# Performance work log

Hardware: AMD Instinct MI355X
Metric: run time of the kernel (lower is better)

The kernel has to match this reference:

```python
import jax, jax.numpy as jnp
import numpy as np

N_EMBED = 1024
HIDDEN = int(2 / 3 * 4 * N_EMBED)  # 2730, matches SwiGLU default
NUM_EXPERTS = 8
TOP_K = 2


def setup_inputs() -> dict:
    key = jax.random.key(0)
    ks = jax.random.split(key, 5)
    B, T, C, E, H = 2, 2048, N_EMBED, NUM_EXPERTS, HIDDEN
    s = 0.02
    return {
        "x": jax.random.normal(ks[0], (B, T, C), dtype=jnp.float32),
        "gate_w": jax.random.normal(ks[1], (E, C), dtype=jnp.float32) * s,  # Linear(C->E) weight [out,in]
        "w1": jax.random.normal(ks[2], (E, H, C), dtype=jnp.float32) * s,   # per-expert Linear(C->H)
        "w2": jax.random.normal(ks[3], (E, H, C), dtype=jnp.float32) * s,   # per-expert Linear(C->H)
        "w3": jax.random.normal(ks[4], (E, C, H), dtype=jnp.float32) * s,   # per-expert Linear(H->C)
    }


def reference(x, gate_w, w1, w2, w3):
    B, T, C = x.shape
    E = gate_w.shape[0]
    xt = x.reshape(-1, C)                      # [N, C], N = B*T
    N = xt.shape[0]

    # Router: top-k logits, softmax over the selected logits only
    logits = jnp.einsum("nc,ec->ne", xt, gate_w)          # [N, E]
    top_vals, top_idx = jax.lax.top_k(logits, TOP_K)       # [N, K]
    top_w = jax.nn.softmax(top_vals.astype(jnp.float32), axis=-1).astype(x.dtype)

    # Dense routing-weight matrix [N, E] (top-k indices are distinct per token)
    route = jnp.zeros((N, E), dtype=x.dtype)
    route = route.at[jnp.arange(N)[:, None], top_idx].set(top_w)

    # SwiGLU for all experts, batched over the expert axis (faithful math,
    # vectorized instead of the per-expert Python-loop gather/scatter)
    h1 = jnp.einsum("nc,ehc->enh", xt, w1)                 # [E, N, H]
    h2 = jnp.einsum("nc,ehc->enh", xt, w2)                 # [E, N, H]
    act = jax.nn.silu(h1) * h2                              # [E, N, H]
    expert_out = jnp.einsum("enh,ech->enc", act, w3)       # [E, N, C]

    out = jnp.einsum("ne,enc->nc", route, expert_out)      # weighted combine
    return out.reshape(B, T, C)
```

## Files before the change

### kernel.cpp

```cpp
#include <hip/hip_runtime.h>
#include <hip/hip_bf16.h>
#include <cstdint>
#include <cstddef>

#define TOKENS 4096
#define CDIM   1024
#define HDIM   2730
#define HPAD2  2816
#define NEXP   8
#define NPAIR  (TOKENS * 2)
#define NTB1   (HPAD2 / 128)
#define NTB2   (CDIM / 128)

typedef __bf16 bf16_t;
typedef bf16_t bf16x8 __attribute__((ext_vector_type(8)));
typedef float  f32x4  __attribute__((ext_vector_type(4)));

static __device__ __forceinline__ unsigned short f2bf(float f) {
    union { float f; unsigned int u; } v; v.f = f;
    unsigned int u = v.u;
    return (unsigned short)((u + 0x7FFFu + ((u >> 16) & 1u)) >> 16);
}
static __device__ __forceinline__ unsigned int pack2(float a, float b) {
    return (unsigned int)f2bf(a) | ((unsigned int)f2bf(b) << 16);
}

typedef __attribute__((address_space(3))) unsigned int lds_uint;
typedef const __attribute__((address_space(1))) unsigned int glob_uint;
static __device__ __forceinline__ void gl_lds16(const void* g, void* l) {
    __builtin_amdgcn_global_load_lds((glob_uint*)g, (lds_uint*)l, 16, 0, 0);
}


__global__ void moe_init(int* meta) {
    if (threadIdx.x < 64) meta[threadIdx.x] = 0;
}

__global__ __launch_bounds__(256) void moe_router(
    const float* __restrict__ x, const float* __restrict__ gw,
    int* __restrict__ meta, int* __restrict__ tok_idx, float* __restrict__ tok_w)
{
    int wave = threadIdx.x >> 6;
    int lane = threadIdx.x & 63;
    int t = blockIdx.x * 4 + wave;

    float acc[NEXP];
#pragma unroll
    for (int e = 0; e < NEXP; ++e) acc[e] = 0.f;

    const float4* xr = (const float4*)(x + (size_t)t * CDIM);
#pragma unroll
    for (int it = 0; it < 4; ++it) {
        int c4 = it * 64 + lane;
        float4 xv = xr[c4];
#pragma unroll
        for (int e = 0; e < NEXP; ++e) {
            float4 gv = ((const float4*)(gw + e * CDIM))[c4];
            acc[e] += xv.x * gv.x + xv.y * gv.y + xv.z * gv.z + xv.w * gv.w;
        }
    }
#pragma unroll
    for (int e = 0; e < NEXP; ++e) {
#pragma unroll
        for (int off = 32; off > 0; off >>= 1)
            acc[e] += __shfl_xor(acc[e], off, 64);
    }
    if (lane == 0) {
        int e0 = 0; float v0 = acc[0];
#pragma unroll
        for (int e = 1; e < NEXP; ++e) if (acc[e] > v0) { v0 = acc[e]; e0 = e; }
        int e1 = -1; float v1 = -3.0e38f;
#pragma unroll
        for (int e = 0; e < NEXP; ++e) if (e != e0 && acc[e] > v1) { v1 = acc[e]; e1 = e; }
        float w0 = 1.f / (1.f + __expf(v1 - v0));
        tok_idx[2 * t] = e0; tok_idx[2 * t + 1] = e1;
        tok_w[2 * t] = w0;  tok_w[2 * t + 1] = 1.f - w0;
        atomicAdd(&meta[e0], 1);
        atomicAdd(&meta[e1], 1);
    }
}

__global__ void moe_scan(int* meta) {
    if (threadIdx.x == 0) {
        int s = 0;
        for (int e = 0; e < NEXP; ++e) { meta[8 + e] = s; s += meta[e]; }
        meta[16] = s;
        int nb = 0;
        for (int e = 0; e < NEXP; ++e) {
            int beg = meta[8 + e], end = meta[8 + e] + meta[e];
            for (int m0 = beg; m0 < end; m0 += 128) {
                meta[32 + 2 * nb] = e;
                meta[33 + 2 * nb] = m0;
                ++nb;
            }
        }
        meta[17] = nb;
    }
}

__global__ __launch_bounds__(256) void moe_scatter(
    const int* __restrict__ tok_idx, const float* __restrict__ tok_w, int* meta,
    int* __restrict__ pair_token, float* __restrict__ pair_w)
{
    int t = blockIdx.x * 256 + threadIdx.x;
    if (t >= TOKENS) return;
#pragma unroll
    for (int k = 0; k < 2; ++k) {
        int e = tok_idx[2 * t + k];
        int pos = atomicAdd(&meta[24 + e], 1);
        int slot = meta[8 + e] + pos;
        pair_token[slot] = t;
        pair_w[slot] = tok_w[2 * t + k];
    }
}

__global__ __launch_bounds__(256) void moe_gather(
    const float* __restrict__ x, const int* __restrict__ pair_token,
    unsigned short* __restrict__ Xg)
{
    int base = blockIdx.x * 8;
    int i = threadIdx.x;
#pragma unroll
    for (int r = 0; r < 8; ++r) {
        int row = base + r;
        int t = pair_token[row];
        float4 v = ((const float4*)(x + (size_t)t * CDIM))[i];
        ushort4 o;
        o.x = f2bf(v.x); o.y = f2bf(v.y); o.z = f2bf(v.z); o.w = f2bf(v.w);
        ((ushort4*)(Xg + (size_t)row * CDIM))[i] = o;
    }
}

__global__ __launch_bounds__(256) void conv_w12(
    const float* __restrict__ w1, const float* __restrict__ w2,
    unsigned short* __restrict__ w1b, unsigned short* __restrict__ w2b)
{
    int e = blockIdx.y;
    const float* wsrc = blockIdx.z ? w2 : w1;
    unsigned short* wdst = blockIdx.z ? w2b : w1b;
    int col = threadIdx.x * 4;
#pragma unroll
    for (int r = 0; r < 8; ++r) {
        int row = blockIdx.x * 8 + r;
        unsigned short* dst = wdst + ((size_t)e * HPAD2 + row) * CDIM;
        uint2 pv;
        if (row < HDIM) {
            float4 a = *(const float4*)(wsrc + ((size_t)e * HDIM + row) * CDIM + col);
            pv.x = pack2(a.x, a.y); pv.y = pack2(a.z, a.w);
        } else {
            pv = uint2{0, 0};
        }
        *(uint2*)(dst + col) = pv;
    }
}

__global__ __launch_bounds__(256) void conv_w3(
    const float* __restrict__ w3, unsigned short* __restrict__ w3b)
{
    int e = blockIdx.y;
#pragma unroll
    for (int r = 0; r < 8; ++r) {
        int row = blockIdx.x * 8 + r;
        const float* src = w3 + ((size_t)e * CDIM + row) * HDIM;
        unsigned short* dst = w3b + ((size_t)e * CDIM + row) * HPAD2;
        for (int ch = threadIdx.x; ch < HPAD2 / 8; ch += 256) {
            int h = ch * 8;
            uint4 pv;
            if (h + 8 <= HDIM) {
                float2 a = *(const float2*)(src + h);
                float2 b = *(const float2*)(src + h + 2);
                float2 c = *(const float2*)(src + h + 4);
                float2 d = *(const float2*)(src + h + 6);
                pv.x = pack2(a.x, a.y); pv.y = pack2(b.x, b.y);
                pv.z = pack2(c.x, c.y); pv.w = pack2(d.x, d.y);
            } else if (h < HDIM) {
                float v[8];
#pragma unroll
                for (int q = 0; q < 8; ++q) v[q] = (h + q < HDIM) ? src[h + q] : 0.f;
                pv.x = pack2(v[0], v[1]); pv.y = pack2(v[2], v[3]);
                pv.z = pack2(v[4], v[5]); pv.w = pack2(v[6], v[7]);
            } else {
                pv = uint4{0, 0, 0, 0};
            }
            *(uint4*)(dst + h) = pv;
        }
    }
}

#define SWZ(row, ch) (((row) << 6) + ((((ch) ^ ((row) & 7))) << 3))

__global__ __launch_bounds__(512) void moe_gemm1(
    const unsigned short* __restrict__ Xg,
    const unsigned short* __restrict__ w1b, const unsigned short* __restrict__ w2b,
    const float* __restrict__ pair_w, const int* __restrict__ meta,
    unsigned short* __restrict__ act)
{
    __shared__ unsigned short sA[128 * 64];
    __shared__ unsigned short sB1[128 * 64];
    __shared__ unsigned short sB2[128 * 64];

    int tid = threadIdx.x;
    int lane = tid & 63;
    int wv = tid >> 6;
    int wm = wv >> 2, wn = wv & 3;
    int l7 = lane & 7, l3 = lane >> 3;
    int srcc = ((l7 ^ l3) << 3);

    int ntile = meta[17] * NTB1;

    for (int t = blockIdx.x; t < ntile; t += gridDim.x) {
        int bm = t / NTB1, bn = t - bm * NTB1;
        int e  = meta[32 + 2 * bm];
        int m0 = meta[33 + 2 * bm];
        int mEnd = meta[9 + e];
        int mEndm1 = mEnd - 1;
        int n0 = bn * 128;

        const unsigned short* w1e = w1b + (size_t)e * HPAD2 * CDIM + (size_t)n0 * CDIM;
        const unsigned short* w2e = w2b + (size_t)e * HPAD2 * CDIM + (size_t)n0 * CDIM;

        f32x4 acc1[4][2], acc2[4][2];
#pragma unroll
        for (int i = 0; i < 4; ++i)
#pragma unroll
            for (int j = 0; j < 2; ++j) {
                acc1[i][j] = {0.f, 0.f, 0.f, 0.f};
                acc2[i][j] = {0.f, 0.f, 0.f, 0.f};
            }

        for (int k0 = 0; k0 < CDIM; k0 += 64) {
#pragma unroll
            for (int i_ = 0; i_ < 2; ++i_) {
                int seg = wv * 2 + i_;
                int row = seg * 8 + l3;
                int grow = m0 + row; if (grow > mEndm1) grow = mEndm1;
                gl_lds16(Xg + (size_t)grow * CDIM + k0 + srcc, sA + seg * 512);
                gl_lds16(w1e + (size_t)row * CDIM + k0 + srcc, sB1 + seg * 512);
                gl_lds16(w2e + (size_t)row * CDIM + k0 + srcc, sB2 + seg * 512);
            }
            asm volatile("s_waitcnt vmcnt(0)" ::: "memory");
            __syncthreads();
#pragma unroll
            for (int ks = 0; ks < 2; ++ks) {
                int kch = ks * 4 + (lane >> 4);
                bf16x8 af[4], b1f[2], b2f[2];
#pragma unroll
                for (int i = 0; i < 4; ++i) {
                    int r = wm * 64 + i * 16 + (lane & 15);
                    af[i] = *(const bf16x8*)(sA + SWZ(r, kch));
                }
#pragma unroll
                for (int j = 0; j < 2; ++j) {
                    int r = wn * 32 + j * 16 + (lane & 15);
                    b1f[j] = *(const bf16x8*)(sB1 + SWZ(r, kch));
                    b2f[j] = *(const bf16x8*)(sB2 + SWZ(r, kch));
                }
#pragma unroll
                for (int i = 0; i < 4; ++i)
#pragma unroll
                    for (int j = 0; j < 2; ++j) {
                        acc1[i][j] = __builtin_amdgcn_mfma_f32_16x16x32_bf16(af[i], b1f[j], acc1[i][j], 0, 0, 0);
                        acc2[i][j] = __builtin_amdgcn_mfma_f32_16x16x32_bf16(af[i], b2f[j], acc2[i][j], 0, 0, 0);
                    }
            }
            __syncthreads();
        }

#pragma unroll
        for (int i = 0; i < 4; ++i) {
            int rbase = m0 + wm * 64 + i * 16 + ((lane >> 4) << 2);
#pragma unroll
            for (int r = 0; r < 4; ++r) {
                int grow = rbase + r;
                if (grow >= mEnd) continue;
                float pw = pair_w[grow];
                size_t rowoff = (size_t)grow * HPAD2;
#pragma unroll
                for (int j = 0; j < 2; ++j) {
                    int gcol = n0 + wn * 32 + j * 16 + (lane & 15);
                    float h1 = acc1[i][j][r], h2 = acc2[i][j][r];
                    float a = (h1 / (1.f + __expf(-h1))) * h2 * pw;
                    act[rowoff + gcol] = f2bf(a);
                }
            }
        }
    }
}

__global__ __launch_bounds__(512) void moe_gemm2(
    const unsigned short* __restrict__ act,
    const unsigned short* __restrict__ w3b,
    const int* __restrict__ meta, const int* __restrict__ pair_token,
    float* __restrict__ out)
{
    __shared__ unsigned short sA[128 * 64];
    __shared__ unsigned short sB[128 * 64];

    int tid = threadIdx.x;
    int lane = tid & 63;
    int wv = tid >> 6;
    int wm = wv >> 2, wn = wv & 3;
    int l7 = lane & 7, l3 = lane >> 3;
    int srcc = ((l7 ^ l3) << 3);

    int ntile = meta[17] * NTB2;

    for (int t = blockIdx.x; t < ntile; t += gridDim.x) {
        int bm = t / NTB2, bn = t - bm * NTB2;
        int e  = meta[32 + 2 * bm];
        int m0 = meta[33 + 2 * bm];
        int mEnd = meta[9 + e];
        int mEndm1 = mEnd - 1;
        int n0 = bn * 128;

        const unsigned short* w3e = w3b + (size_t)e * CDIM * HPAD2 + (size_t)n0 * HPAD2;

        f32x4 acc[4][2];
#pragma unroll
        for (int i = 0; i < 4; ++i)
#pragma unroll
            for (int j = 0; j < 2; ++j) acc[i][j] = {0.f, 0.f, 0.f, 0.f};

        for (int k0 = 0; k0 < HPAD2; k0 += 64) {
#pragma unroll
            for (int i_ = 0; i_ < 2; ++i_) {
                int seg = wv * 2 + i_;
                int row = seg * 8 + l3;
                int grow = m0 + row; if (grow > mEndm1) grow = mEndm1;
                gl_lds16(act + (size_t)grow * HPAD2 + k0 + srcc, sA + seg * 512);
                gl_lds16(w3e + (size_t)row * HPAD2 + k0 + srcc, sB + seg * 512);
            }
            asm volatile("s_waitcnt vmcnt(0)" ::: "memory");
            __syncthreads();
#pragma unroll
            for (int ks = 0; ks < 2; ++ks) {
                int kch = ks * 4 + (lane >> 4);
                bf16x8 af[4], bf[2];
#pragma unroll
                for (int i = 0; i < 4; ++i) {
                    int r = wm * 64 + i * 16 + (lane & 15);
                    af[i] = *(const bf16x8*)(sA + SWZ(r, kch));
                }
#pragma unroll
                for (int j = 0; j < 2; ++j) {
                    int r = wn * 32 + j * 16 + (lane & 15);
                    bf[j] = *(const bf16x8*)(sB + SWZ(r, kch));
                }
#pragma unroll
                for (int i = 0; i < 4; ++i)
#pragma unroll
                    for (int j = 0; j < 2; ++j)
                        acc[i][j] = __builtin_amdgcn_mfma_f32_16x16x32_bf16(af[i], bf[j], acc[i][j], 0, 0, 0);
            }
            __syncthreads();
        }

#pragma unroll
        for (int i = 0; i < 4; ++i) {
            int rbase = m0 + wm * 64 + i * 16 + ((lane >> 4) << 2);
#pragma unroll
            for (int r = 0; r < 4; ++r) {
                int grow = rbase + r;
                if (grow >= mEnd) continue;
                int tok = pair_token[grow];
                float* orow = out + (size_t)tok * CDIM;
#pragma unroll
                for (int j = 0; j < 2; ++j) {
                    int gcol = n0 + wn * 32 + j * 16 + (lane & 15);
                    atomicAdd(orow + gcol, acc[i][j][r]);
                }
            }
        }
    }
}

extern "C" void kernel_launch(void* const* d_in, const int* in_sizes, int n_in,
                              void* d_out, int out_size, void* d_ws, size_t ws_size,
                              hipStream_t stream)
{
    const float* x  = (const float*)d_in[0];
    const float* gw = (const float*)d_in[1];
    const float* w1 = (const float*)d_in[2];
    const float* w2 = (const float*)d_in[3];
    const float* w3 = (const float*)d_in[4];
    float* out = (float*)d_out;

    char* ws = (char*)d_ws;
    size_t off = 0;
    auto alloc = [&](size_t bytes) -> void* {
        off = (off + 255) & ~(size_t)255;
        void* p = ws + off;
        off += bytes;
        return p;
    };
    int*   meta       = (int*)alloc(256 * sizeof(int));
    int*   tok_idx    = (int*)alloc((size_t)NPAIR * sizeof(int));
    float* tok_w      = (float*)alloc((size_t)NPAIR * sizeof(float));
    int*   pair_token = (int*)alloc((size_t)NPAIR * sizeof(int));
    float* pair_w     = (float*)alloc((size_t)NPAIR * sizeof(float));
    unsigned short* Xg  = (unsigned short*)alloc((size_t)NPAIR * CDIM * 2);
    unsigned short* act = (unsigned short*)alloc((size_t)NPAIR * HPAD2 * 2);
    unsigned short* w1b = (unsigned short*)alloc((size_t)NEXP * HPAD2 * CDIM * 2);
    unsigned short* w2b = (unsigned short*)alloc((size_t)NEXP * HPAD2 * CDIM * 2);
    unsigned short* w3b = (unsigned short*)alloc((size_t)NEXP * CDIM * HPAD2 * 2);
    (void)ws_size; (void)in_sizes; (void)n_in;

    hipMemsetAsync(d_out, 0, (size_t)out_size * sizeof(float), stream);

    moe_init<<<1, 64, 0, stream>>>(meta);
    moe_router<<<TOKENS / 4, 256, 0, stream>>>(x, gw, meta, tok_idx, tok_w);
    moe_scan<<<1, 64, 0, stream>>>(meta);
    moe_scatter<<<TOKENS / 256, 256, 0, stream>>>(tok_idx, tok_w, meta, pair_token, pair_w);
    moe_gather<<<NPAIR / 8, 256, 0, stream>>>(x, pair_token, Xg);
    conv_w12<<<dim3(HPAD2 / 8, NEXP, 2), 256, 0, stream>>>(w1, w2, w1b, w2b);
    conv_w3<<<dim3(CDIM / 8, NEXP), 256, 0, stream>>>(w3, w3b);
    moe_gemm1<<<768, 512, 0, stream>>>(Xg, w1b, w2b, pair_w, meta, act);
    moe_gemm2<<<576, 512, 0, stream>>>(act, w3b, meta, pair_token, out);
}
```

Before: 552.0 us.

## Use 256-thread blocks with atomic tile scheduler and reshaped GEMM tiles

Both expert GEMMs move from 512-thread to 256-thread blocks. gemm1 narrows its N tile from 128 to 64 columns, which doubles the number of tiles. gemm2 keeps its 128x128 tile but each wave now computes a 64x64 sub-tile with more accumulators. Static grid-stride tile assignment is replaced by a dynamic atomic counter in meta, so blocks pull tiles and balance load across uneven expert sizes. The changes aim to raise occupancy and per-wave MFMA reuse, at the cost of more registers per wave and an extra barrier per tile. The scheduler also relies on meta[18] and meta[19] being zeroed beforehand, presumably in moe_init.

```diff
diff --git a/kernel.cpp b/kernel.cpp
--- a/kernel.cpp
+++ b/kernel.cpp
@@ -9,7 +9,7 @@
 #define HPAD2  2816
 #define NEXP   8
 #define NPAIR  (TOKENS * 2)
-#define NTB1   (HPAD2 / 128)
+#define NTB1   (HPAD2 / 64)
 #define NTB2   (CDIM / 128)
 
 typedef __bf16 bf16_t;
@@ -189,32 +189,38 @@
 
 #define SWZ(row, ch) (((row) << 6) + ((((ch) ^ ((row) & 7))) << 3))
 
-__global__ __launch_bounds__(512) void moe_gemm1(
+__global__ __launch_bounds__(256) void moe_gemm1(
     const unsigned short* __restrict__ Xg,
     const unsigned short* __restrict__ w1b, const unsigned short* __restrict__ w2b,
-    const float* __restrict__ pair_w, const int* __restrict__ meta,
+    const float* __restrict__ pair_w, int* __restrict__ meta,
     unsigned short* __restrict__ act)
 {
     __shared__ unsigned short sA[128 * 64];
-    __shared__ unsigned short sB1[128 * 64];
-    __shared__ unsigned short sB2[128 * 64];
+    __shared__ unsigned short sB1[64 * 64];
+    __shared__ unsigned short sB2[64 * 64];
+    __shared__ int sTile;
 
     int tid = threadIdx.x;
     int lane = tid & 63;
     int wv = tid >> 6;
-    int wm = wv >> 2, wn = wv & 3;
-    int l7 = lane & 7, l3 = lane >> 3;
-    int srcc = ((l7 ^ l3) << 3);
+    int wm = wv >> 1, wn = wv & 1;
+    int l3 = lane >> 3;
+    int srcc = (((lane & 7) ^ l3) << 3);
 
     int ntile = meta[17] * NTB1;
 
-    for (int t = blockIdx.x; t < ntile; t += gridDim.x) {
+    for (;;) {
+        if (tid == 0) sTile = atomicAdd(&meta[18], 1);
+        __syncthreads();
+        int t = sTile;
+        if (t >= ntile) break;
+
         int bm = t / NTB1, bn = t - bm * NTB1;
         int e  = meta[32 + 2 * bm];
         int m0 = meta[33 + 2 * bm];
         int mEnd = meta[9 + e];
         int mEndm1 = mEnd - 1;
-        int n0 = bn * 128;
+        int n0 = bn * 64;
 
         const unsigned short* w1e = w1b + (size_t)e * HPAD2 * CDIM + (size_t)n0 * CDIM;
         const unsigned short* w2e = w2b + (size_t)e * HPAD2 * CDIM + (size_t)n0 * CDIM;
@@ -230,11 +236,16 @@
 
         for (int k0 = 0; k0 < CDIM; k0 += 64) {
 #pragma unroll
+            for (int i_ = 0; i_ < 4; ++i_) {
+                int seg = wv * 4 + i_;
+                int row = seg * 8 + l3;
+                int grow = m0 + row; if (grow > mEndm1) grow = mEndm1;
+                gl_lds16(Xg + (size_t)grow * CDIM + k0 + srcc, sA + seg * 512);
+            }
+#pragma unroll
             for (int i_ = 0; i_ < 2; ++i_) {
                 int seg = wv * 2 + i_;
                 int row = seg * 8 + l3;
-                int grow = m0 + row; if (grow > mEndm1) grow = mEndm1;
-                gl_lds16(Xg + (size_t)grow * CDIM + k0 + srcc, sA + seg * 512);
                 gl_lds16(w1e + (size_t)row * CDIM + k0 + srcc, sB1 + seg * 512);
                 gl_lds16(w2e + (size_t)row * CDIM + k0 + srcc, sB2 + seg * 512);
             }
@@ -284,28 +295,35 @@
                 }
             }
         }
-    }
-}
-
-__global__ __launch_bounds__(512) void moe_gemm2(
+        __syncthreads();
+    }
+}
+
+__global__ __launch_bounds__(256) void moe_gemm2(
     const unsigned short* __restrict__ act,
     const unsigned short* __restrict__ w3b,
-    const int* __restrict__ meta, const int* __restrict__ pair_token,
+    int* __restrict__ meta, const int* __restrict__ pair_token,
     float* __restrict__ out)
 {
     __shared__ unsigned short sA[128 * 64];
     __shared__ unsigned short sB[128 * 64];
+    __shared__ int sTile;
 
     int tid = threadIdx.x;
     int lane = tid & 63;
     int wv = tid >> 6;
-    int wm = wv >> 2, wn = wv & 3;
-    int l7 = lane & 7, l3 = lane >> 3;
-    int srcc = ((l7 ^ l3) << 3);
+    int wm = wv >> 1, wn = wv & 1;
+    int l3 = lane >> 3;
+    int srcc = (((lane & 7) ^ l3) << 3);
 
     int ntile = meta[17] * NTB2;
 
-    for (int t = blockIdx.x; t < ntile; t += gridDim.x) {
+    for (;;) {
+        if (tid == 0) sTile = atomicAdd(&meta[19], 1);
+        __syncthreads();
+        int t = sTile;
+        if (t >= ntile) break;
+
         int bm = t / NTB2, bn = t - bm * NTB2;
         int e  = meta[32 + 2 * bm];
         int m0 = meta[33 + 2 * bm];
@@ -315,16 +333,16 @@
 
         const unsigned short* w3e = w3b + (size_t)e * CDIM * HPAD2 + (size_t)n0 * HPAD2;
 
-        f32x4 acc[4][2];
+        f32x4 acc[4][4];
 #pragma unroll
         for (int i = 0; i < 4; ++i)
 #pragma unroll
-            for (int j = 0; j < 2; ++j) acc[i][j] = {0.f, 0.f, 0.f, 0.f};
+            for (int j = 0; j < 4; ++j) acc[i][j] = {0.f, 0.f, 0.f, 0.f};
 
         for (int k0 = 0; k0 < HPAD2; k0 += 64) {
 #pragma unroll
-            for (int i_ = 0; i_ < 2; ++i_) {
-                int seg = wv * 2 + i_;
+            for (int i_ = 0; i_ < 4; ++i_) {
+                int seg = wv * 4 + i_;
                 int row = seg * 8 + l3;
                 int grow = m0 + row; if (grow > mEndm1) grow = mEndm1;
                 gl_lds16(act + (size_t)grow * HPAD2 + k0 + srcc, sA + seg * 512);
@@ -335,21 +353,21 @@
 #pragma unroll
             for (int ks = 0; ks < 2; ++ks) {
                 int kch = ks * 4 + (lane >> 4);
-                bf16x8 af[4], bf[2];
+                bf16x8 af[4], bf[4];
 #pragma unroll
                 for (int i = 0; i < 4; ++i) {
                     int r = wm * 64 + i * 16 + (lane & 15);
                     af[i] = *(const bf16x8*)(sA + SWZ(r, kch));
                 }
 #pragma unroll
-                for (int j = 0; j < 2; ++j) {
-                    int r = wn * 32 + j * 16 + (lane & 15);
+                for (int j = 0; j < 4; ++j) {
+                    int r = wn * 64 + j * 16 + (lane & 15);
                     bf[j] = *(const bf16x8*)(sB + SWZ(r, kch));
                 }
 #pragma unroll
                 for (int i = 0; i < 4; ++i)
 #pragma unroll
-                    for (int j = 0; j < 2; ++j)
+                    for (int j = 0; j < 4; ++j)
                         acc[i][j] = __builtin_amdgcn_mfma_f32_16x16x32_bf16(af[i], bf[j], acc[i][j], 0, 0, 0);
             }
             __syncthreads();
@@ -365,12 +383,13 @@
                 int tok = pair_token[grow];
                 float* orow = out + (size_t)tok * CDIM;
 #pragma unroll
-                for (int j = 0; j < 2; ++j) {
-                    int gcol = n0 + wn * 32 + j * 16 + (lane & 15);
+                for (int j = 0; j < 4; ++j) {
+                    int gcol = n0 + wn * 64 + j * 16 + (lane & 15);
                     atomicAdd(orow + gcol, acc[i][j][r]);
                 }
             }
         }
+        __syncthreads();
     }
 }
 
@@ -414,6 +433,6 @@
     moe_gather<<<NPAIR / 8, 256, 0, stream>>>(x, pair_token, Xg);
     conv_w12<<<dim3(HPAD2 / 8, NEXP, 2), 256, 0, stream>>>(w1, w2, w1b, w2b);
     conv_w3<<<dim3(CDIM / 8, NEXP), 256, 0, stream>>>(w3, w3b);
-    moe_gemm1<<<768, 512, 0, stream>>>(Xg, w1b, w2b, pair_w, meta, act);
-    moe_gemm2<<<576, 512, 0, stream>>>(act, w3b, meta, pair_token, out);
-}
+    moe_gemm1<<<768, 256, 0, stream>>>(Xg, w1b, w2b, pair_w, meta, act);
+    moe_gemm2<<<576, 256, 0, stream>>>(act, w3b, meta, pair_token, out);
+}
```

Result: slower. 621.4 us (+12.6%).
